# Kernel optimization log

Hardware: AMD Instinct MI355X
Metric: run time of the kernel (lower is better)

Reference implementation:

```python
import jax, jax.numpy as jnp
import numpy as np

N = 50000
E = 1600000
D_IN = 128
D_HID = 128
K = 16  # n_clusters


def spmm(edge_index, edge_weight, feats):
    # out[i] = sum_{(i<-j) in edges} w_e * feats[j]
    dst, src = edge_index[0], edge_index[1]
    msgs = feats[src] * edge_weight[:, None]  # [E, d]
    return jax.ops.segment_sum(msgs, dst, num_segments=N)


def gcn_with_skip(x, edge_index, edge_weight, W, b, skip_w):
    transformed = x @ W + b                      # Linear kernel
    propagated = spmm(edge_index, edge_weight, transformed)
    return jax.nn.selu(skip_w * transformed + propagated)


def setup_inputs() -> dict:
    key = jax.random.key(0)
    ks = jax.random.split(key, 12)
    x = jax.random.normal(ks[0], (N, D_IN), dtype=jnp.float32)
    edge_index = jax.random.randint(ks[1], (2, E), 0, N, dtype=jnp.int32)
    edge_weight = jax.random.uniform(ks[2], (E,), dtype=jnp.float32)
    s1 = 1.0 / np.sqrt(D_IN)
    s2 = 1.0 / np.sqrt(D_HID)
    W1 = jax.random.uniform(ks[3], (D_IN, D_HID), jnp.float32, -s1, s1)
    b1 = jax.random.uniform(ks[4], (D_HID,), jnp.float32, -s1, s1)
    skip1 = jnp.ones((D_HID,), jnp.float32)
    W2 = jax.random.uniform(ks[5], (D_HID, D_HID), jnp.float32, -s2, s2)
    b2 = jax.random.uniform(ks[6], (D_HID,), jnp.float32, -s2, s2)
    skip2 = jnp.ones((D_HID,), jnp.float32)
    Wa = jax.random.uniform(ks[7], (D_HID, K), jnp.float32, -s2, s2)
    ba = jax.random.uniform(ks[8], (K,), jnp.float32, -s2, s2)
    return {"x": x, "edge_index": edge_index, "edge_weight": edge_weight,
            "W1": W1, "b1": b1, "skip1": skip1,
            "W2": W2, "b2": b2, "skip2": skip2,
            "Wa": Wa, "ba": ba}


def reference(x, edge_index, edge_weight, W1, b1, skip1, W2, b2, skip2, Wa, ba):
    h = gcn_with_skip(x, edge_index, edge_weight, W1, b1, skip1)
    h = gcn_with_skip(h, edge_index, edge_weight, W2, b2, skip2)
    assignments = jax.nn.softmax(h @ Wa + ba, axis=-1)  # [N, K]
    return assignments
```

## Files before the change

kernel.cpp:

```cpp
#include <hip/hip_runtime.h>
#include <hip/hip_bf16.h>
#include <hip/hip_fp16.h>

#define NN 50000
#define NE 1600000
#define DD 128
#define KC 16

#define NB 3125
#define NBP (NB + 1)
#define CHUNK 6144
#define NCHUNK 261
#define BT 1024
#define EPT 6
#define MAXB 768
#define SB 784

#define GEMM_BLKS 391

typedef __attribute__((ext_vector_type(8))) short s8v;
typedef __attribute__((ext_vector_type(4))) float f4v;
typedef __attribute__((ext_vector_type(2))) float f2v;

__device__ __forceinline__ f2v up2(unsigned u) {
    f2v r;
    r.x = __uint_as_float(u << 16);
    r.y = __uint_as_float(u & 0xFFFF0000u);
    return r;
}
__device__ __forceinline__ float wof(unsigned rec) {
    return __half2float(__ushort_as_half((unsigned short)(rec >> 16)));
}


__device__ __forceinline__ void wprep_one(const float* __restrict__ W, s8v* __restrict__ Wf, int g) {
    int l = g & 63;
    int kcnt = g >> 6;
    int kc = kcnt >> 3, nt = kcnt & 7;
    int n = nt * 16 + (l & 15);
    int kb = kc * 32 + (l >> 4) * 8;
    union { s8v v; __hip_bfloat162 h2[4]; } u;
    #pragma unroll
    for (int q = 0; q < 4; q++) {
        float lo = W[(size_t)(kb + 2 * q) * 128 + n];
        float hi = W[(size_t)(kb + 2 * q + 1) * 128 + n];
        u.h2[q] = __float22bfloat162_rn(make_float2(lo, hi));
    }
    Wf[(size_t)kcnt * 64 + l] = u.v;
}


__global__ __launch_bounds__(BT) void k_binprep(const int* __restrict__ dst,
                                                const int* __restrict__ src,
                                                const float* __restrict__ w,
                                                int2* __restrict__ staging2,
                                                unsigned short* __restrict__ offs,
                                                const float* __restrict__ W1,
                                                const float* __restrict__ W2,
                                                s8v* __restrict__ Wf1,
                                                s8v* __restrict__ Wf2) {
    __shared__ int cnt[NB];
    __shared__ int s[BT];
    int t = threadIdx.x;
    int bid = blockIdx.x;

    if (bid >= NCHUNK) {
        int idx = bid - NCHUNK;
        int g = (idx & 1) * 1024 + t;
        if (idx < 2) wprep_one(W1, Wf1, g);
        else         wprep_one(W2, Wf2, g);
        return;
    }

    int c = bid;
    size_t cbase = (size_t)c * CHUNK;
    for (int i = t; i < NB; i += BT) cnt[i] = 0;
    __syncthreads();

    int dreg[EPT], sreg[EPT]; float wreg[EPT];
    #pragma unroll
    for (int j = 0; j < EPT; j++) {
        size_t e = cbase + j * BT + t;
        bool ok = e < NE;
        size_t ee = ok ? e : (NE - 1);
        dreg[j] = dst[ee]; sreg[j] = src[ee]; wreg[j] = w[ee];
        if (!ok) dreg[j] = -1;
        if (ok) atomicAdd(&cnt[dreg[j] >> 4], 1);
    }
    __syncthreads();

    int v[4]; int sum = 0;
    #pragma unroll
    for (int j = 0; j < 4; j++) { int i = t * 4 + j; v[j] = (i < NB) ? cnt[i] : 0; sum += v[j]; }
    s[t] = sum; __syncthreads();
    for (int off = 1; off < BT; off <<= 1) {
        int u = (t >= off) ? s[t - off] : 0;
        __syncthreads();
        s[t] += u;
        __syncthreads();
    }
    int run = (t == 0) ? 0 : s[t - 1];
    #pragma unroll
    for (int j = 0; j < 4; j++) {
        int i = t * 4 + j;
        if (i < NB) { offs[(size_t)c * NBP + i] = (unsigned short)run; cnt[i] = run; run += v[j]; }
    }
    if (t == BT - 1) offs[(size_t)c * NBP + NB] = (unsigned short)s[BT - 1];
    __syncthreads();

    #pragma unroll
    for (int j = 0; j < EPT; j++) {
        if (dreg[j] >= 0) {
            int b = dreg[j] >> 4;
            int li = atomicAdd(&cnt[b], 1);
            staging2[cbase + li] = make_int2(((dreg[j] & 15) << 16) | sreg[j],
                                            __float_as_int(wreg[j]));
        }
    }
}


__device__ __forceinline__ s8v load_afrag(const float* p) {
    union { s8v v; __hip_bfloat162 h2[4]; } a;
    float4 f0 = *(const float4*)p;
    float4 f1 = *(const float4*)(p + 4);
    a.h2[0] = __float22bfloat162_rn(make_float2(f0.x, f0.y));
    a.h2[1] = __float22bfloat162_rn(make_float2(f0.z, f0.w));
    a.h2[2] = __float22bfloat162_rn(make_float2(f1.x, f1.y));
    a.h2[3] = __float22bfloat162_rn(make_float2(f1.z, f1.w));
    return a.v;
}
__device__ __forceinline__ s8v load_afrag(const __hip_bfloat16* p) {
    return *(const s8v*)p;
}

template <typename TI>
__device__ __forceinline__ void gemm_body(const TI* __restrict__ X,
                                          const s8v* __restrict__ Wf,
                                          const float* __restrict__ bias,
                                          __hip_bfloat16* __restrict__ Out,
                                          int nrows, int wave, int lane) {
    int m0 = wave * 32;
    if (m0 >= nrows) return;
    int col = lane & 15;
    int quad = lane >> 4;

    f4v acc[2][8];
    #pragma unroll
    for (int mt = 0; mt < 2; mt++)
        #pragma unroll
        for (int nt = 0; nt < 8; nt++) acc[mt][nt] = (f4v){0.f, 0.f, 0.f, 0.f};

    int row0 = m0 + col;
    int row1 = m0 + 16 + col;
    if (row0 >= nrows) row0 = nrows - 1;
    if (row1 >= nrows) row1 = nrows - 1;
    const TI* xr0 = X + (size_t)row0 * 128 + quad * 8;
    const TI* xr1 = X + (size_t)row1 * 128 + quad * 8;

    #pragma unroll 1
    for (int kc = 0; kc < 4; kc++) {
        s8v a0 = load_afrag(xr0 + kc * 32);
        s8v a1 = load_afrag(xr1 + kc * 32);
        #pragma unroll
        for (int nt = 0; nt < 8; nt++) {
            s8v b = Wf[(size_t)(kc * 8 + nt) * 64 + lane];
            acc[0][nt] = __builtin_amdgcn_mfma_f32_16x16x32_bf16(a0, b, acc[0][nt], 0, 0, 0);
            acc[1][nt] = __builtin_amdgcn_mfma_f32_16x16x32_bf16(a1, b, acc[1][nt], 0, 0, 0);
        }
    }

    float bb[8];
    #pragma unroll
    for (int nt = 0; nt < 8; nt++) bb[nt] = bias[nt * 16 + col];

    #pragma unroll
    for (int mt = 0; mt < 2; mt++) {
        #pragma unroll
        for (int r = 0; r < 4; r++) {
            int row = m0 + mt * 16 + quad * 4 + r;
            if (row < nrows) {
                __hip_bfloat16* orow = Out + (size_t)row * 128 + col;
                #pragma unroll
                for (int nt = 0; nt < 8; nt++) {
                    orow[nt * 16] = __float2bfloat16(acc[mt][nt][r] + bb[nt]);
                }
            }
        }
    }
}


__global__ __launch_bounds__(256) void k_sortgemm(const int2* __restrict__ staging2,
                                                  const unsigned short* __restrict__ offs,
                                                  unsigned* __restrict__ staging4,
                                                  int* __restrict__ rowptr,
                                                  const float* __restrict__ x,
                                                  const s8v* __restrict__ Wf1,
                                                  const float* __restrict__ b1,
                                                  __hip_bfloat16* __restrict__ T) {
    __shared__ int2 ebuf[MAXB];
    __shared__ unsigned srec[MAXB];
    __shared__ int segoff[NCHUNK + 1];
    __shared__ int cstart[NCHUNK];
    __shared__ int s2[256];
    __shared__ int rcnt[16];
    __shared__ int rowoff[17];
    int bid = blockIdx.x, t = threadIdx.x;

    if (bid >= NB) {
        int wave = (bid - NB) * 4 + (t >> 6);
        gemm_body<float>(x, Wf1, b1, T, NN, wave, t & 63);
        return;
    }

    int b = bid;
    for (int c = t; c < NCHUNK; c += 256) {
        int o0 = offs[(size_t)c * NBP + b];
        int o1 = offs[(size_t)c * NBP + b + 1];
        cstart[c] = o0;
        segoff[c] = o1 - o0;
    }
    __syncthreads();
    int a0 = (2 * t < NCHUNK) ? segoff[2 * t] : 0;
    int a1 = (2 * t + 1 < NCHUNK) ? segoff[2 * t + 1] : 0;
    s2[t] = a0 + a1; __syncthreads();
    for (int off = 1; off < 256; off <<= 1) {
        int u = (t >= off) ? s2[t - off] : 0;
        __syncthreads();
        s2[t] += u;
        __syncthreads();
    }
    int base0 = (t == 0) ? 0 : s2[t - 1];
    int total = s2[255];
    __syncthreads();
    if (2 * t < NCHUNK) segoff[2 * t] = base0;
    if (2 * t + 1 < NCHUNK) segoff[2 * t + 1] = base0 + a0;
    if (t == 0) segoff[NCHUNK] = total;
    __syncthreads();

    int cnt = total; if (cnt > MAXB) cnt = MAXB;

    for (int i = t; i < cnt; i += 256) {
        int lo = 0, hi = NCHUNK;
        while (hi - lo > 1) {
            int mid = (lo + hi) >> 1;
            if (segoff[mid] <= i) lo = mid; else hi = mid;
        }
        ebuf[i] = staging2[(size_t)lo * CHUNK + cstart[lo] + (i - segoff[lo])];
    }
    __syncthreads();

    if (t < 16) rcnt[t] = 0;
    __syncthreads();
    for (int i = t; i < cnt; i += 256) atomicAdd(&rcnt[(unsigned)ebuf[i].x >> 16], 1);
    __syncthreads();
    if (t < 16) {
        int v = rcnt[t];
        int p = v;
        #pragma unroll
        for (int off = 1; off < 16; off <<= 1) {
            int u = __shfl_up(p, off, 64);
            if (t >= off) p += u;
        }
        rowoff[t] = p - v;
        if (t == 15) rowoff[16] = p;
        rcnt[t] = p - v;
    }
    __syncthreads();
    for (int i = t; i < cnt; i += 256) {
        int2 rec = ebuf[i];
        int p = atomicAdd(&rcnt[(unsigned)rec.x >> 16], 1);
        unsigned hb = __half_as_ushort(__float2half_rn(__int_as_float(rec.y)));
        srec[p] = ((unsigned)rec.x & 0xFFFFu) | (hb << 16);
    }
    __syncthreads();

    unsigned* outp = staging4 + (size_t)b * SB;
    for (int i = t; i < cnt; i += 256) outp[i] = srec[i];
    if (t < 8) outp[cnt + t] = 0u;
    if (t < 17) rowptr[b * 17 + t] = rowoff[t];
}


__global__ __launch_bounds__(256) void k_gemm2(const __hip_bfloat16* __restrict__ X,
                                               const s8v* __restrict__ Wf,
                                               const float* __restrict__ bias,
                                               __hip_bfloat16* __restrict__ Out) {
    int wave = blockIdx.x * 4 + (threadIdx.x >> 6);
    gemm_body<__hip_bfloat16>(X, Wf, bias, Out, NN, wave, threadIdx.x & 63);
}


template <int ASSIGN>
__global__ __launch_bounds__(256) void k_spmm(const __hip_bfloat16* __restrict__ T,
                                              const unsigned* __restrict__ staging4,
                                              const int* __restrict__ rowptr,
                                              const float* __restrict__ skip,
                                              __hip_bfloat16* __restrict__ Hout,
                                              const float* __restrict__ Wa,
                                              const float* __restrict__ ba,
                                              float* __restrict__ aout) {
    __shared__ __align__(16) unsigned srec[MAXB + 16];
    __shared__ int rowoff[17];
    int b = blockIdx.x;
    int tid = threadIdx.x;

    if (tid < 17) rowoff[tid] = rowptr[b * 17 + tid];
    __syncthreads();
    int cnt = rowoff[16];
    int nv4 = (cnt + 11) >> 2;
    const uint4* sp4 = (const uint4*)(staging4 + (size_t)b * SB);
    for (int i = tid; i < nv4; i += 256) ((uint4*)srec)[i] = sp4[i];
    __syncthreads();

    int wv = tid >> 6, lane = tid & 63;
    int q = lane >> 4;
    int fk = lane & 15;
    const int4* Tv4 = (const int4*)T;

    float sk[8];
    *(float4*)&sk[0] = *(const float4*)(skip + fk * 8);
    *(float4*)&sk[4] = *(const float4*)(skip + fk * 8 + 4);

    float wreg[32];
    float bav[4];
    if (ASSIGN) {
        #pragma unroll
        for (int j = 0; j < 8; j++)
            *(float4*)&wreg[j * 4] = *(const float4*)(Wa + (size_t)(8 * fk + j) * KC + 4 * q);
        #pragma unroll
        for (int c = 0; c < 4; c++) bav[c] = ba[4 * q + c];
    }

    const float scale = 1.0507009873554805f, alpha = 1.6732632423543772f;

    for (int r = wv; r < 16; r += 4) {
        int g = b * 16 + r;
        int o = rowoff[r], oe = rowoff[r + 1];
        f2v a01 = (f2v){0.f, 0.f}, a23 = (f2v){0.f, 0.f};
        f2v a45 = (f2v){0.f, 0.f}, a67 = (f2v){0.f, 0.f};

        for (; o + 16 <= oe; o += 16) {
            unsigned c0 = srec[o + q];
            unsigned c1 = srec[o + 4 + q];
            unsigned c2 = srec[o + 8 + q];
            unsigned c3 = srec[o + 12 + q];
            int4 t0 = Tv4[(size_t)(c0 & 0xFFFFu) * 16 + fk];
            int4 t1 = Tv4[(size_t)(c1 & 0xFFFFu) * 16 + fk];
            int4 t2 = Tv4[(size_t)(c2 & 0xFFFFu) * 16 + fk];
            int4 t3 = Tv4[(size_t)(c3 & 0xFFFFu) * 16 + fk];
            float w0 = wof(c0), w1 = wof(c1), w2 = wof(c2), w3 = wof(c3);
            a01 += w0 * up2(t0.x); a23 += w0 * up2(t0.y);
            a45 += w0 * up2(t0.z); a67 += w0 * up2(t0.w);
            a01 += w1 * up2(t1.x); a23 += w1 * up2(t1.y);
            a45 += w1 * up2(t1.z); a67 += w1 * up2(t1.w);
            a01 += w2 * up2(t2.x); a23 += w2 * up2(t2.y);
            a45 += w2 * up2(t2.z); a67 += w2 * up2(t2.w);
            a01 += w3 * up2(t3.x); a23 += w3 * up2(t3.y);
            a45 += w3 * up2(t3.z); a67 += w3 * up2(t3.w);
        }
        for (; o + 8 <= oe; o += 8) {
            unsigned c0 = srec[o + q];
            unsigned c1 = srec[o + 4 + q];
            int4 t0 = Tv4[(size_t)(c0 & 0xFFFFu) * 16 + fk];
            int4 t1 = Tv4[(size_t)(c1 & 0xFFFFu) * 16 + fk];
            float w0 = wof(c0), w1 = wof(c1);
            a01 += w0 * up2(t0.x); a23 += w0 * up2(t0.y);
            a45 += w0 * up2(t0.z); a67 += w0 * up2(t0.w);
            a01 += w1 * up2(t1.x); a23 += w1 * up2(t1.y);
            a45 += w1 * up2(t1.z); a67 += w1 * up2(t1.w);
        }
        for (; o < oe; o += 4) {
            int i0 = o + q;
            unsigned c0 = srec[i0];
            int4 t0 = Tv4[(size_t)(c0 & 0xFFFFu) * 16 + fk];
            float w0 = (i0 < oe) ? wof(c0) : 0.f;
            a01 += w0 * up2(t0.x); a23 += w0 * up2(t0.y);
            a45 += w0 * up2(t0.z); a67 += w0 * up2(t0.w);
        }

        float acc[8];
        acc[0] = a01.x; acc[1] = a01.y; acc[2] = a23.x; acc[3] = a23.y;
        acc[4] = a45.x; acc[5] = a45.y; acc[6] = a67.x; acc[7] = a67.y;
        #pragma unroll
        for (int j = 0; j < 8; j++) {
            acc[j] += __shfl_xor(acc[j], 16, 64);
            acc[j] += __shfl_xor(acc[j], 32, 64);
        }

        int4 ts = Tv4[(size_t)g * 16 + fk];
        f2v s01 = up2(ts.x), s23 = up2(ts.y), s45 = up2(ts.z), s67 = up2(ts.w);
        float v[8];
        v[0] = sk[0] * s01.x + acc[0]; v[1] = sk[1] * s01.y + acc[1];
        v[2] = sk[2] * s23.x + acc[2]; v[3] = sk[3] * s23.y + acc[3];
        v[4] = sk[4] * s45.x + acc[4]; v[5] = sk[5] * s45.y + acc[5];
        v[6] = sk[6] * s67.x + acc[6]; v[7] = sk[7] * s67.y + acc[7];
        #pragma unroll
        for (int j = 0; j < 8; j++)
            v[j] = scale * (v[j] > 0.f ? v[j] : alpha * (__expf(v[j]) - 1.f));

        if (!ASSIGN) {
            if (q == 0) {
                union { int4 i4; __hip_bfloat162 h2[4]; } pk;
                #pragma unroll
                for (int j = 0; j < 4; j++)
                    pk.h2[j] = __float22bfloat162_rn(make_float2(v[2 * j], v[2 * j + 1]));
                *(int4*)(Hout + (size_t)g * 128 + fk * 8) = pk.i4;
            }
        } else {
            float p4[4] = {0.f, 0.f, 0.f, 0.f};
            #pragma unroll
            for (int j = 0; j < 8; j++)
                #pragma unroll
                for (int c = 0; c < 4; c++) p4[c] += v[j] * wreg[j * 4 + c];
            #pragma unroll
            for (int off = 1; off <= 8; off <<= 1)
                #pragma unroll
                for (int c = 0; c < 4; c++) p4[c] += __shfl_xor(p4[c], off, 64);
            #pragma unroll
            for (int c = 0; c < 4; c++) p4[c] += bav[c];
            float m = fmaxf(fmaxf(p4[0], p4[1]), fmaxf(p4[2], p4[3]));
            m = fmaxf(m, __shfl_xor(m, 16, 64));
            m = fmaxf(m, __shfl_xor(m, 32, 64));
            float e0 = __expf(p4[0] - m), e1 = __expf(p4[1] - m);
            float e2 = __expf(p4[2] - m), e3 = __expf(p4[3] - m);
            float s = e0 + e1 + e2 + e3;
            s += __shfl_xor(s, 16, 64);
            s += __shfl_xor(s, 32, 64);
            if (fk < 4) {
                float ev = e0;
                ev = (fk == 1) ? e1 : ev;
                ev = (fk == 2) ? e2 : ev;
                ev = (fk == 3) ? e3 : ev;
                aout[(size_t)g * KC + 4 * q + fk] = ev / s;
            }
        }
    }
}


extern "C" void kernel_launch(void* const* d_in, const int* in_sizes, int n_in,
                              void* d_out, int out_size, void* d_ws, size_t ws_size,
                              hipStream_t stream) {
    const float* x     = (const float*)d_in[0];
    const int*   eidx  = (const int*)d_in[1];
    const float* ew    = (const float*)d_in[2];
    const float* W1    = (const float*)d_in[3];
    const float* b1    = (const float*)d_in[4];
    const float* skip1 = (const float*)d_in[5];
    const float* W2    = (const float*)d_in[6];
    const float* b2    = (const float*)d_in[7];
    const float* skip2 = (const float*)d_in[8];
    const float* Wa    = (const float*)d_in[9];
    const float* ba    = (const float*)d_in[10];
    float* out = (float*)d_out;

    const int* dst = eidx;
    const int* src = eidx + NE;

    char* ws = (char*)d_ws;
    size_t off = 0;
    __hip_bfloat16* T = (__hip_bfloat16*)(ws + off);  off += (size_t)NN * DD * 2;
    __hip_bfloat16* Hb = (__hip_bfloat16*)(ws + off); off += (size_t)NN * DD * 2;
    int2* staging2 = (int2*)(ws + off);               off += (size_t)NCHUNK * CHUNK * 8;
    unsigned* staging4 = (unsigned*)(ws + off);       off += (size_t)NB * SB * 4;
    unsigned short* offs = (unsigned short*)(ws + off); off += (size_t)NCHUNK * NBP * 2;
    int* rowptr = (int*)(ws + off);                   off += (size_t)NB * 17 * 4;
    s8v* Wf1 = (s8v*)(ws + off);                      off += 2048 * 16;
    s8v* Wf2 = (s8v*)(ws + off);                      off += 2048 * 16;

    k_binprep<<<NCHUNK + 4, BT, 0, stream>>>(dst, src, ew, staging2, offs, W1, W2, Wf1, Wf2);
    k_sortgemm<<<NB + GEMM_BLKS, 256, 0, stream>>>(staging2, offs, staging4, rowptr,
                                                   x, Wf1, b1, T);
    k_spmm<0><<<NB, 256, 0, stream>>>(T, staging4, rowptr, skip1, Hb, nullptr, nullptr, nullptr);
    k_gemm2<<<GEMM_BLKS, 256, 0, stream>>>(Hb, Wf2, b2, T);
    k_spmm<1><<<NB, 256, 0, stream>>>(T, staging4, rowptr, skip2, nullptr, Wa, ba, out);
}
```

Before: 261.9 us.

## Fuse second linear layer GEMM into first SpMM epilogue via LDS-staged MFMA

The first SpMM kernel now stages its 16 SELU output rows per block in shared memory and multiplies them by W2 with bf16 MFMA, writing the transformed features straight to a new buffer. This removes the separate GEMM launch and the global write and read of the intermediate hidden matrix. In exchange, each SpMM block does extra MFMA work plus a block-wide barrier. The output stores are scalar bf16 writes scattered per column, which may coalesce worse than the old GEMM's stores.

```diff
diff --git a/kernel.cpp b/kernel.cpp
--- a/kernel.cpp
+++ b/kernel.cpp
@@ -17,6 +17,7 @@
 #define SB 784
 
 #define GEMM_BLKS 391
+#define HB_LD 136
 
 typedef __attribute__((ext_vector_type(8))) short s8v;
 typedef __attribute__((ext_vector_type(4))) float f4v;
@@ -129,9 +130,6 @@
     a.h2[2] = __float22bfloat162_rn(make_float2(f1.x, f1.y));
     a.h2[3] = __float22bfloat162_rn(make_float2(f1.z, f1.w));
     return a.v;
-}
-__device__ __forceinline__ s8v load_afrag(const __hip_bfloat16* p) {
-    return *(const s8v*)p;
 }
 
 template <typename TI>
@@ -283,26 +281,20 @@
 }
 
 
-__global__ __launch_bounds__(256) void k_gemm2(const __hip_bfloat16* __restrict__ X,
-                                               const s8v* __restrict__ Wf,
-                                               const float* __restrict__ bias,
-                                               __hip_bfloat16* __restrict__ Out) {
-    int wave = blockIdx.x * 4 + (threadIdx.x >> 6);
-    gemm_body<__hip_bfloat16>(X, Wf, bias, Out, NN, wave, threadIdx.x & 63);
-}
-
-
-template <int ASSIGN>
+template <int MODE>
 __global__ __launch_bounds__(256) void k_spmm(const __hip_bfloat16* __restrict__ T,
                                               const unsigned* __restrict__ staging4,
                                               const int* __restrict__ rowptr,
                                               const float* __restrict__ skip,
-                                              __hip_bfloat16* __restrict__ Hout,
+                                              const s8v* __restrict__ Wfb,
+                                              const float* __restrict__ bias2,
+                                              __hip_bfloat16* __restrict__ T2,
                                               const float* __restrict__ Wa,
                                               const float* __restrict__ ba,
                                               float* __restrict__ aout) {
     __shared__ __align__(16) unsigned srec[MAXB + 16];
     __shared__ int rowoff[17];
+    __shared__ __align__(16) __hip_bfloat16 hbuf[(MODE == 0) ? (16 * HB_LD) : 8];
     int b = blockIdx.x;
     int tid = threadIdx.x;
 
@@ -325,7 +317,7 @@
 
     float wreg[32];
     float bav[4];
-    if (ASSIGN) {
+    if (MODE == 1) {
         #pragma unroll
         for (int j = 0; j < 8; j++)
             *(float4*)&wreg[j * 4] = *(const float4*)(Wa + (size_t)(8 * fk + j) * KC + 4 * q);
@@ -400,13 +392,13 @@
         for (int j = 0; j < 8; j++)
             v[j] = scale * (v[j] > 0.f ? v[j] : alpha * (__expf(v[j]) - 1.f));
 
-        if (!ASSIGN) {
+        if (MODE == 0) {
             if (q == 0) {
                 union { int4 i4; __hip_bfloat162 h2[4]; } pk;
                 #pragma unroll
                 for (int j = 0; j < 4; j++)
                     pk.h2[j] = __float22bfloat162_rn(make_float2(v[2 * j], v[2 * j + 1]));
-                *(int4*)(Hout + (size_t)g * 128 + fk * 8) = pk.i4;
+                *(int4*)&hbuf[r * HB_LD + fk * 8] = pk.i4;
             }
         } else {
             float p4[4] = {0.f, 0.f, 0.f, 0.f};
@@ -437,6 +429,32 @@
             }
         }
     }
+
+    if (MODE == 0) {
+        __syncthreads();
+        int col = fk;
+        int quad = q;
+        int nt0 = wv * 2, nt1 = nt0 + 1;
+        f4v acc0 = (f4v){0.f, 0.f, 0.f, 0.f};
+        f4v acc1 = (f4v){0.f, 0.f, 0.f, 0.f};
+        #pragma unroll
+        for (int kc = 0; kc < 4; kc++) {
+            s8v a = *(const s8v*)&hbuf[col * HB_LD + kc * 32 + quad * 8];
+            s8v b0 = Wfb[(size_t)(kc * 8 + nt0) * 64 + lane];
+            s8v b1 = Wfb[(size_t)(kc * 8 + nt1) * 64 + lane];
+            acc0 = __builtin_amdgcn_mfma_f32_16x16x32_bf16(a, b0, acc0, 0, 0, 0);
+            acc1 = __builtin_amdgcn_mfma_f32_16x16x32_bf16(a, b1, acc1, 0, 0, 0);
+        }
+        float bb0 = bias2[nt0 * 16 + col];
+        float bb1 = bias2[nt1 * 16 + col];
+        #pragma unroll
+        for (int r4 = 0; r4 < 4; r4++) {
+            int grow = b * 16 + quad * 4 + r4;
+            __hip_bfloat16* orow = T2 + (size_t)grow * 128;
+            orow[nt0 * 16 + col] = __float2bfloat16(acc0[r4] + bb0);
+            orow[nt1 * 16 + col] = __float2bfloat16(acc1[r4] + bb1);
+        }
+    }
 }
 
 
@@ -461,8 +479,8 @@
 
     char* ws = (char*)d_ws;
     size_t off = 0;
-    __hip_bfloat16* T = (__hip_bfloat16*)(ws + off);  off += (size_t)NN * DD * 2;
-    __hip_bfloat16* Hb = (__hip_bfloat16*)(ws + off); off += (size_t)NN * DD * 2;
+    __hip_bfloat16* T  = (__hip_bfloat16*)(ws + off); off += (size_t)NN * DD * 2;
+    __hip_bfloat16* T2 = (__hip_bfloat16*)(ws + off); off += (size_t)NN * DD * 2;
     int2* staging2 = (int2*)(ws + off);               off += (size_t)NCHUNK * CHUNK * 8;
     unsigned* staging4 = (unsigned*)(ws + off);       off += (size_t)NB * SB * 4;
     unsigned short* offs = (unsigned short*)(ws + off); off += (size_t)NCHUNK * NBP * 2;
@@ -473,7 +491,8 @@
     k_binprep<<<NCHUNK + 4, BT, 0, stream>>>(dst, src, ew, staging2, offs, W1, W2, Wf1, Wf2);
     k_sortgemm<<<NB + GEMM_BLKS, 256, 0, stream>>>(staging2, offs, staging4, rowptr,
                                                    x, Wf1, b1, T);
-    k_spmm<0><<<NB, 256, 0, stream>>>(T, staging4, rowptr, skip1, Hb, nullptr, nullptr, nullptr);
-    k_gemm2<<<GEMM_BLKS, 256, 0, stream>>>(Hb, Wf2, b2, T);
-    k_spmm<1><<<NB, 256, 0, stream>>>(T, staging4, rowptr, skip2, nullptr, Wa, ba, out);
-}
+    k_spmm<0><<<NB, 256, 0, stream>>>(T, staging4, rowptr, skip1,
+                                      Wf2, b2, T2, nullptr, nullptr, nullptr);
+    k_spmm<1><<<NB, 256, 0, stream>>>(T2, staging4, rowptr, skip2,
+                                      nullptr, nullptr, nullptr, Wa, ba, out);
+}
```

Result: faster. 250.0 us (-4.6%).
